# Kernel tuning notes

Hardware: AMD Instinct MI355X
Metric: run time of the kernel (lower is better)

Reference implementation:

```python
import jax, jax.numpy as jnp
import numpy as np

WIN_SIZE = 11
SIGMA = 1.5
WEIGHTS = np.array([0.0448, 0.2856, 0.3001, 0.2363, 0.1333], dtype=np.float32)
K1, K2 = 0.01, 0.03
DATA_RANGE = 255.0
C1 = (K1 * DATA_RANGE) ** 2
C2 = (K2 * DATA_RANGE) ** 2
N_SCALES = 5


def _gauss1d():
    coords = np.arange(WIN_SIZE, dtype=np.float32) - WIN_SIZE // 2
    g = np.exp(-(coords ** 2) / (2.0 * SIGMA ** 2))
    g /= g.sum()
    return jnp.asarray(g, dtype=jnp.float32)


def _blur(x, g):
    # separable depthwise gaussian blur, VALID padding (matches pytorch_msssim)
    C = x.shape[1]
    wh = jnp.tile(g.reshape(1, 1, 1, WIN_SIZE), (C, 1, 1, 1))
    wv = jnp.tile(g.reshape(1, 1, WIN_SIZE, 1), (C, 1, 1, 1))
    dn = ('NCHW', 'OIHW', 'NCHW')
    x = jax.lax.conv_general_dilated(x, wh, (1, 1), 'VALID', dimension_numbers=dn, feature_group_count=C)
    x = jax.lax.conv_general_dilated(x, wv, (1, 1), 'VALID', dimension_numbers=dn, feature_group_count=C)
    return x


def _ssim(X, Y, g):
    mu1 = _blur(X, g)
    mu2 = _blur(Y, g)
    mu1_sq = mu1 * mu1
    mu2_sq = mu2 * mu2
    mu1_mu2 = mu1 * mu2
    sigma1_sq = _blur(X * X, g) - mu1_sq
    sigma2_sq = _blur(Y * Y, g) - mu2_sq
    sigma12 = _blur(X * Y, g) - mu1_mu2
    cs_map = (2.0 * sigma12 + C2) / (sigma1_sq + sigma2_sq + C2)
    ssim_map = ((2.0 * mu1_mu2 + C1) / (mu1_sq + mu2_sq + C1)) * cs_map
    return ssim_map.mean(axis=(2, 3)), cs_map.mean(axis=(2, 3))  # [B,C] each


def _avg_pool2(x):
    # avg_pool2d kernel=2 stride=2; H,W chosen even at every scale so padding=0
    return jax.lax.reduce_window(x, 0.0, jax.lax.add, (1, 1, 2, 2), (1, 1, 2, 2), 'VALID') / 4.0


def setup_inputs() -> dict:
    key = jax.random.key(0)
    k1, k2 = jax.random.split(key)
    shape = (32, 3, 384, 384)
    prediction = jax.random.uniform(k1, shape, dtype=jnp.float32) * DATA_RANGE
    truth = jax.random.uniform(k2, shape, dtype=jnp.float32) * DATA_RANGE
    return {"prediction": prediction, "truth": truth}


def reference(prediction, truth):
    g = _gauss1d()
    w = jnp.asarray(WEIGHTS)
    X, Y = prediction, truth
    mcs = []
    for i in range(N_SCALES):
        ssim_pc, cs = _ssim(X, Y, g)
        if i < N_SCALES - 1:
            mcs.append(jax.nn.relu(cs))
            X = _avg_pool2(X)
            Y = _avg_pool2(Y)
    vals = jnp.stack(mcs + [jax.nn.relu(ssim_pc)], axis=0)  # [5,B,C]
    ms_ssim_val = jnp.prod(vals ** w.reshape(-1, 1, 1), axis=0)  # [B,C]
    return 1.0 - ms_ssim_val.mean()
```

## Files before the change

### kernel.cpp

```cpp
#include <hip/hip_runtime.h>
#include <math.h>


namespace {

constexpr int NIMG = 96;
constexpr float TWO_C1 = 13.005f;
constexpr float TWO_C2 = 117.045f;

__device__ constexpr float GW[11] = {
    0.00102838f, 0.00759875f, 0.03600077f, 0.10936070f, 0.21300553f,
    0.26601172f,
    0.21300553f, 0.10936070f, 0.03600077f, 0.00759875f, 0.00102838f};

typedef float f2 __attribute__((ext_vector_type(2)));
typedef float f4 __attribute__((ext_vector_type(4)));

__device__ __forceinline__ f2 pk_mul(f2 a, f2 b) {
  f2 d;
  asm("v_pk_mul_f32 %0, %1, %2" : "=v"(d) : "v"(a), "v"(b));
  return d;
}
__device__ __forceinline__ f2 pk_mul_s1lo(f2 a, f2 b) {
  f2 d;
  asm("v_pk_mul_f32 %0, %1, %2 op_sel:[0,0] op_sel_hi:[1,0]"
      : "=v"(d) : "v"(a), "v"(b));
  return d;
}
__device__ __forceinline__ void fma_w(f2& d, f2 q, f2 p) {
  asm("v_pk_fma_f32 %0, %1, %2, %0 op_sel:[0,0,0] op_sel_hi:[0,1,1]"
      : "+v"(d) : "v"(q), "v"(p));
}
__device__ __forceinline__ void fma_nl(f2& d, f2 q, f2 t) {
  asm("v_pk_fma_f32 %0, %1, %2, %0 op_sel:[0,0,0] op_sel_hi:[1,0,1]"
      : "+v"(d) : "v"(q), "v"(t));
}
__device__ __forceinline__ void fma_nh(f2& d, f2 q, f2 t) {
  asm("v_pk_fma_f32 %0, %1, %2, %0 op_sel:[0,1,0] op_sel_hi:[1,1,1]"
      : "+v"(d) : "v"(q), "v"(t));
}
__device__ __forceinline__ void fma_sl(f2& d, f2 q, f2 t) {
  asm("v_pk_fma_f32 %0, %1, %2, %0 op_sel:[1,0,0] op_sel_hi:[0,0,1]"
      : "+v"(d) : "v"(q), "v"(t));
}
__device__ __forceinline__ void fma_sh(f2& d, f2 q, f2 t) {
  asm("v_pk_fma_f32 %0, %1, %2, %0 op_sel:[1,1,0] op_sel_hi:[0,1,1]"
      : "+v"(d) : "v"(q), "v"(t));
}

__device__ __forceinline__ float wshl1(float v) {
  return __int_as_float(__builtin_amdgcn_mov_dpp(
      __float_as_int(v), 0x130, 0xF, 0xF, true));
}
__device__ __forceinline__ f2 wshl1v(f2 v) {
  f2 r;
  r.x = wshl1(v.x);
  r.y = wshl1(v.y);
  return r;
}

struct SPtrs {
  const float* ip[4];
};

template <bool BASE, bool CLAMP>
__device__ __forceinline__ void vblur(const float* __restrict__ XP,
                                      const float* __restrict__ YP, int row0,
                                      int W2, int H, int cp, f2 (&AU)[4],
                                      f2 (&AW)[4], f2 (&BU)[4], f2 (&BW)[4],
                                      const f2 (&QQ)[6]) {
  const f2* PA = (const f2*)XP;
  const f2* PB = (const f2*)YP;
  const f4* PV = (const f4*)XP;
  f2 sa[14], sb[14];
  f4 sv[14];
#pragma unroll
  for (int j = 0; j < 14; ++j) {
    int rin = row0 + j;
    if (CLAMP) rin = rin < H - 1 ? rin : H - 1;
    const int off = rin * W2 + cp;
    if (BASE) {
      sa[j] = PA[off];
      sb[j] = PB[off];
    } else {
      sv[j] = PV[off];
    }
  }
  __builtin_amdgcn_sched_barrier(0);
#pragma unroll
  for (int j = 0; j < 14; ++j) {
    f2 Pu, Pw;
    if (BASE) {
      f2 pa = sa[j], pb = sb[j];
      Pu = pa + pb;
      Pw = pa - pb;
    } else {
      f4 v = sv[j];
      Pu.x = v.x; Pu.y = v.y;
      Pw.x = v.z; Pw.y = v.w;
    }
    f2 Qu = pk_mul(Pu, Pu), Qw = pk_mul(Pw, Pw);
#pragma unroll
    for (int i = 0; i < 4; ++i) {
      const int k = j - i;
      if (k >= 0 && k <= 10) {
        const int qi = k <= 5 ? k : 10 - k;
        fma_w(AU[i], QQ[qi], Pu);
        fma_w(AW[i], QQ[qi], Pw);
        fma_w(BU[i], QQ[qi], Qu);
        fma_w(BW[i], QQ[qi], Qw);
      }
    }
  }
}

template <bool BASE>
__device__ __forceinline__ void ssim_tile(const float* __restrict__ XP,
                                          const float* __restrict__ YP,
                                          int H, int x0, int tw, int by,
                                          int s, int img,
                                          float* __restrict__ acc) {
  __shared__ float red[2][4];
  const int W2 = H >> 1, OH = H - 10;
  const int t = threadIdx.x;
  const int lane = t & 63, wv = t >> 6;
  int cp = (x0 >> 1) + lane;
  cp = cp < W2 - 1 ? cp : W2 - 1;
  const int row0 = by * 16 + wv * 4;

  f2 QQ[6];
  QQ[0].x = GW[0]; QQ[0].y = 0.f;
#pragma unroll
  for (int n = 1; n < 6; ++n) { QQ[n].x = GW[n]; QQ[n].y = GW[n - 1]; }

  float ssim_s = 0.f, cs_s = 0.f;

  if (row0 < OH) {
    f2 AU[4] = {}, AW[4] = {}, BU[4] = {}, BW[4] = {};
    const bool noclamp = (row0 + 13 <= H - 1);
    if (noclamp) vblur<BASE, false>(XP, YP, row0, W2, H, cp, AU, AW, BU, BW, QQ);
    else         vblur<BASE, true >(XP, YP, row0, W2, H, cp, AU, AW, BU, BW, QQ);

    auto hb = [&QQ](f2 tt) -> f2 {
      f2 h = pk_mul_s1lo(QQ[0], tt);
      fma_nh(h, QQ[1], tt);
      tt = wshl1v(tt);
      fma_nl(h, QQ[2], tt);
      fma_nh(h, QQ[3], tt);
      tt = wshl1v(tt);
      fma_nl(h, QQ[4], tt);
      fma_nh(h, QQ[5], tt);
      tt = wshl1v(tt);
      fma_sl(h, QQ[5], tt);
      fma_sh(h, QQ[4], tt);
      tt = wshl1v(tt);
      fma_sl(h, QQ[3], tt);
      fma_sh(h, QQ[2], tt);
      tt = wshl1v(tt);
      fma_sl(h, QQ[1], tt);
      fma_sh(h, QQ[0], tt);
      return h;
    };

    const bool vx = (2 * lane) < tw;
    const bool vy = (2 * lane + 1) < tw;
#pragma unroll
    for (int i = 0; i < 4; ++i) {
      if (row0 + i < OH) {
        f2 bU = hb(AU[i]), bW = hb(AW[i]);
        f2 bU2 = hb(BU[i]), bW2 = hb(BW[i]);
        f2 m2u = pk_mul(bU, bU), m2w = pk_mul(bW, bW);
        f2 Pm = m2u - m2w;
        f2 Qm = m2u + m2w;
        f2 Am = bU2 - bW2;
        f2 Bm = bU2 + bW2;
        float csx = (Am.x - Pm.x + TWO_C2) *
                    __builtin_amdgcn_rcpf(Bm.x - Qm.x + TWO_C2);
        float lx = (Pm.x + TWO_C1) * __builtin_amdgcn_rcpf(Qm.x + TWO_C1);
        float csy = (Am.y - Pm.y + TWO_C2) *
                    __builtin_amdgcn_rcpf(Bm.y - Qm.y + TWO_C2);
        float ly = (Pm.y + TWO_C1) * __builtin_amdgcn_rcpf(Qm.y + TWO_C1);
        if (vx) { cs_s += csx; ssim_s += lx * csx; }
        if (vy) { cs_s += csy; ssim_s += ly * csy; }
      }
    }
  }

#pragma unroll
  for (int off = 32; off > 0; off >>= 1) {
    ssim_s += __shfl_down(ssim_s, off);
    cs_s += __shfl_down(cs_s, off);
  }
  if (lane == 0) { red[0][wv] = ssim_s; red[1][wv] = cs_s; }
  __syncthreads();
  if (t == 0) {
    atomicAdd(&acc[(2 * s + 0) * NIMG + img],
              red[0][0] + red[0][1] + red[0][2] + red[0][3]);
    atomicAdd(&acc[(2 * s + 1) * NIMG + img],
              red[1][0] + red[1][1] + red[1][2] + red[1][3]);
  }
}

__device__ __forceinline__ void pyramid_body(
    const float* __restrict__ X, const float* __restrict__ Y,
    float* __restrict__ i1, float* __restrict__ i2,
    float* __restrict__ i3, float* __restrict__ i4, int img, int bx) {
  const int t = threadIdx.x;
  const int wv = t >> 6, lane = t & 63;
  const int tidx = bx * 4 + wv;
  const int tx = tidx % 6, ty = tidx / 6;
  const int r = lane >> 4, c = lane & 15;

  const float* Xs = X + (size_t)img * 384 * 384;
  const float* Ys = Y + (size_t)img * 384 * 384;
  f4* p1 = (f4*)i1 + (size_t)img * 192 * 96;
  f4* p2 = (f4*)i2 + (size_t)img * 96 * 48;
  f4* p3 = (f4*)i3 + (size_t)img * 48 * 24;
  f4* p4 = (f4*)i4 + (size_t)img * 24 * 12;

  float h4u = 0.f, h4w = 0.f;
#pragma unroll
  for (int b = 0; b < 2; ++b) {
    const int gr = ty * 16 + b * 8 + 2 * r;
    const int gc = tx * 64 + 4 * c;
    f4 xu = *(const f4*)&Xs[(size_t)gr * 384 + gc];
    f4 xv = *(const f4*)&Xs[(size_t)(gr + 1) * 384 + gc];
    f4 yu = *(const f4*)&Ys[(size_t)gr * 384 + gc];
    f4 yv = *(const f4*)&Ys[(size_t)(gr + 1) * 384 + gc];
    float ax = 0.25f * (xu.x + xu.y + xv.x + xv.y);
    float bx2 = 0.25f * (xu.z + xu.w + xv.z + xv.w);
    float ay = 0.25f * (yu.x + yu.y + yv.x + yv.y);
    float by2 = 0.25f * (yu.z + yu.w + yv.z + yv.w);
    float u0 = ax + ay, u1v = bx2 + by2, w0 = ax - ay, w1v = bx2 - by2;
    {
      f4 st; st.x = u0; st.y = u1v; st.z = w0; st.w = w1v;
      p1[(size_t)(ty * 8 + b * 4 + r) * 96 + tx * 16 + c] = st;
    }
    float hu = u0 + u1v, hw = w0 + w1v;
    float su = 0.25f * (hu + __shfl_xor(hu, 16));
    float sw = 0.25f * (hw + __shfl_xor(hw, 16));
    float suh = __shfl_xor(su, 1), swh = __shfl_xor(sw, 1);
    if ((r & 1) == 0 && (c & 1) == 0) {
      f4 st; st.x = su; st.y = suh; st.z = sw; st.w = swh;
      p2[(size_t)(ty * 4 + 2 * b + (r >> 1)) * 48 + tx * 8 + (c >> 1)] = st;
    }
    float au = su + __shfl_xor(su, 1);
    float aw = sw + __shfl_xor(sw, 1);
    float u3 = 0.25f * (au + __shfl_xor(au, 32));
    float w3 = 0.25f * (aw + __shfl_xor(aw, 32));
    float u3h = __shfl_xor(u3, 2), w3h = __shfl_xor(w3, 2);
    if (r == 0 && (c & 3) == 0) {
      f4 st; st.x = u3; st.y = u3h; st.z = w3; st.w = w3h;
      p3[(size_t)(ty * 2 + b) * 24 + tx * 4 + (c >> 2)] = st;
    }
    float hu4 = u3 + __shfl_xor(u3, 2);
    float hw4 = w3 + __shfl_xor(w3, 2);
    if (b == 0) {
      h4u = hu4; h4w = hw4;
    } else {
      float l4u = 0.25f * (h4u + hu4), l4w = 0.25f * (h4w + hw4);
      float l4uh = __shfl_xor(l4u, 4), l4wh = __shfl_xor(l4w, 4);
      if (r == 0 && (c & 7) == 0) {
        f4 st; st.x = l4u; st.y = l4uh; st.z = l4w; st.w = l4wh;
        p4[(size_t)ty * 12 + tx * 2 + (c >> 3)] = st;
      }
    }
  }
}

__global__ __launch_bounds__(256, 4) void fused_pyr_s0(
    const float* __restrict__ X, const float* __restrict__ Y,
    float* __restrict__ i1, float* __restrict__ i2,
    float* __restrict__ i3, float* __restrict__ i4,
    float* __restrict__ acc) {
  const int img = blockIdx.y;
  if (blockIdx.x < 36) {
    pyramid_body(X, Y, i1, i2, i3, i4, img, blockIdx.x);
    return;
  }
  const int lt = blockIdx.x - 36;
  const int tx = lt & 3, by = lt >> 2;
  const int x0 = tx * 94;
  int tw = 374 - x0;
  tw = tw < 94 ? tw : 94;
  ssim_tile<true>(X + (size_t)img * 384 * 384, Y + (size_t)img * 384 * 384,
                  384, x0, tw, by, 0, img, acc);
}

__global__ __launch_bounds__(256, 4) void ssim_rest(SPtrs sp,
                                                    float* __restrict__ acc) {
  const int img = blockIdx.y;
  const int tile = 96 + blockIdx.x;
  int s;
  if (tile < 120) s = 1;
  else if (tile < 126) s = 2;
  else if (tile < 129) s = 3;
  else s = 4;
  const int tstart[5] = {0, 96, 120, 126, 129};
  const int HH[5] = {384, 192, 96, 48, 24};
  const int NTX[5] = {4, 2, 1, 1, 1};
  const int TWM[5] = {94, 92, 86, 38, 14};
  const int lt = tile - tstart[s];
  const int H = HH[s], OW = H - 10;
  const int tx = lt % NTX[s], by = lt / NTX[s];
  const int x0 = tx * TWM[s];
  const int tw = (TWM[s] < OW - x0) ? TWM[s] : OW - x0;
  const float* XP = sp.ip[s - 1] + (size_t)img * H * (H >> 1) * 4;
  ssim_tile<false>(XP, nullptr, H, x0, tw, by, s, img, acc);
}

__global__ void final_kernel(const float* __restrict__ acc,
                             float* __restrict__ out) {
  __shared__ float prods[NIMG];
  const float wts[5] = {0.0448f, 0.2856f, 0.3001f, 0.2363f, 0.1333f};
  const float inv_npix[5] = {1.f / (374.f * 374.f), 1.f / (182.f * 182.f),
                             1.f / (86.f * 86.f),  1.f / (38.f * 38.f),
                             1.f / (14.f * 14.f)};
  int t = threadIdx.x;
  if (t < NIMG) {
    float p = 1.f;
#pragma unroll
    for (int s = 0; s < 5; ++s) {
      float sum = (s < 4) ? acc[(s * 2 + 1) * NIMG + t]
                          : acc[(s * 2 + 0) * NIMG + t];
      float m = sum * inv_npix[s];
      m = m > 0.f ? m : 0.f;
      p *= powf(m, wts[s]);
    }
    prods[t] = p;
  }
  __syncthreads();
  if (t == 0) {
    float s = 0.f;
    for (int i = 0; i < NIMG; ++i) s += prods[i];
    out[0] = 1.f - s / (float)NIMG;
  }
}

}

extern "C" void kernel_launch(void* const* d_in, const int* in_sizes, int n_in,
                              void* d_out, int out_size, void* d_ws,
                              size_t ws_size, hipStream_t stream) {
  const float* X0 = (const float*)d_in[0];
  const float* Y0 = (const float*)d_in[1];
  float* out = (float*)d_out;
  float* ws = (float*)d_ws;

  const size_t L1 = (size_t)NIMG * 192 * 192 * 2;
  const size_t L2 = (size_t)NIMG * 96 * 96 * 2;
  const size_t L3 = (size_t)NIMG * 48 * 48 * 2;
  const size_t L4 = (size_t)NIMG * 24 * 24 * 2;

  float* i1 = ws;
  float* i2 = i1 + L1;
  float* i3 = i2 + L2;
  float* i4 = i3 + L3;
  float* acc = i4 + L4;

  hipMemsetAsync(acc, 0, 10 * NIMG * sizeof(float), stream);

  fused_pyr_s0<<<dim3(36 + 96, NIMG), dim3(256), 0, stream>>>(
      X0, Y0, i1, i2, i3, i4, acc);

  SPtrs sp;
  sp.ip[0] = i1; sp.ip[1] = i2; sp.ip[2] = i3; sp.ip[3] = i4;

  ssim_rest<<<dim3(34, NIMG), dim3(256), 0, stream>>>(sp, acc);

  final_kernel<<<dim3(1), dim3(128), 0, stream>>>(acc, out);
}
```

Before: 221.3 us.

## Halve vblur load buffer, raise occupancy bound, fold final reduction into last block

The vertical blur now prefetches only 7 rows into registers and refills slots as rows are consumed, instead of preloading all 14. This lowers register pressure so both main kernels can request 5 waves per SIMD instead of 4. The separate final kernel launch is removed: ssim_rest blocks increment an atomic counter, and the last block computes the MS-SSIM product and mean. The smaller prefetch window exposes more load latency, and the tail now depends on atomics and fences working correctly.

```diff
diff --git a/kernel.cpp b/kernel.cpp
--- a/kernel.cpp
+++ b/kernel.cpp
@@ -7,6 +7,7 @@
 constexpr int NIMG = 96;
 constexpr float TWO_C1 = 13.005f;
 constexpr float TWO_C2 = 117.045f;
+constexpr int TOTAL_B = 34 * NIMG;
 
 __device__ constexpr float GW[11] = {
     0.00102838f, 0.00759875f, 0.03600077f, 0.10936070f, 0.21300553f,
@@ -72,10 +73,10 @@
   const f2* PA = (const f2*)XP;
   const f2* PB = (const f2*)YP;
   const f4* PV = (const f4*)XP;
-  f2 sa[14], sb[14];
-  f4 sv[14];
-#pragma unroll
-  for (int j = 0; j < 14; ++j) {
+  f2 sa[7], sb[7];
+  f4 sv[7];
+#pragma unroll
+  for (int j = 0; j < 7; ++j) {
     int rin = row0 + j;
     if (CLAMP) rin = rin < H - 1 ? rin : H - 1;
     const int off = rin * W2 + cp;
@@ -91,13 +92,24 @@
   for (int j = 0; j < 14; ++j) {
     f2 Pu, Pw;
     if (BASE) {
-      f2 pa = sa[j], pb = sb[j];
+      f2 pa = sa[j % 7], pb = sb[j % 7];
       Pu = pa + pb;
       Pw = pa - pb;
     } else {
-      f4 v = sv[j];
+      f4 v = sv[j % 7];
       Pu.x = v.x; Pu.y = v.y;
       Pw.x = v.z; Pw.y = v.w;
+    }
+    if (j + 7 < 14) {
+      int rin = row0 + j + 7;
+      if (CLAMP) rin = rin < H - 1 ? rin : H - 1;
+      const int off = rin * W2 + cp;
+      if (BASE) {
+        sa[j % 7] = PA[off];
+        sb[j % 7] = PB[off];
+      } else {
+        sv[j % 7] = PV[off];
+      }
     }
     f2 Qu = pk_mul(Pu, Pu), Qw = pk_mul(Pw, Pw);
 #pragma unroll
@@ -268,7 +280,7 @@
   }
 }
 
-__global__ __launch_bounds__(256, 4) void fused_pyr_s0(
+__global__ __launch_bounds__(256, 5) void fused_pyr_s0(
     const float* __restrict__ X, const float* __restrict__ Y,
     float* __restrict__ i1, float* __restrict__ i2,
     float* __restrict__ i3, float* __restrict__ i4,
@@ -287,8 +299,10 @@
                   384, x0, tw, by, 0, img, acc);
 }
 
-__global__ __launch_bounds__(256, 4) void ssim_rest(SPtrs sp,
-                                                    float* __restrict__ acc) {
+__global__ __launch_bounds__(256, 5) void ssim_rest(SPtrs sp,
+                                                    float* __restrict__ acc,
+                                                    int* __restrict__ ctr,
+                                                    float* __restrict__ out) {
   const int img = blockIdx.y;
   const int tile = 96 + blockIdx.x;
   int s;
@@ -307,33 +321,41 @@
   const int tw = (TWM[s] < OW - x0) ? TWM[s] : OW - x0;
   const float* XP = sp.ip[s - 1] + (size_t)img * H * (H >> 1) * 4;
   ssim_tile<false>(XP, nullptr, H, x0, tw, by, s, img, acc);
-}
-
-__global__ void final_kernel(const float* __restrict__ acc,
-                             float* __restrict__ out) {
-  __shared__ float prods[NIMG];
-  const float wts[5] = {0.0448f, 0.2856f, 0.3001f, 0.2363f, 0.1333f};
-  const float inv_npix[5] = {1.f / (374.f * 374.f), 1.f / (182.f * 182.f),
-                             1.f / (86.f * 86.f),  1.f / (38.f * 38.f),
-                             1.f / (14.f * 14.f)};
-  int t = threadIdx.x;
-  if (t < NIMG) {
-    float p = 1.f;
-#pragma unroll
-    for (int s = 0; s < 5; ++s) {
-      float sum = (s < 4) ? acc[(s * 2 + 1) * NIMG + t]
-                          : acc[(s * 2 + 0) * NIMG + t];
-      float m = sum * inv_npix[s];
-      m = m > 0.f ? m : 0.f;
-      p *= powf(m, wts[s]);
-    }
-    prods[t] = p;
+
+  const int t = threadIdx.x;
+  __shared__ int sh_last;
+  if (t == 0) {
+    __threadfence();
+    int old = atomicAdd(ctr, 1);
+    sh_last = (old == TOTAL_B - 1) ? 1 : 0;
   }
   __syncthreads();
-  if (t == 0) {
-    float s = 0.f;
-    for (int i = 0; i < NIMG; ++i) s += prods[i];
-    out[0] = 1.f - s / (float)NIMG;
+  if (sh_last) {
+    __threadfence();
+    __shared__ float prods[NIMG];
+    const float wts[5] = {0.0448f, 0.2856f, 0.3001f, 0.2363f, 0.1333f};
+    const float inv_npix[5] = {1.f / (374.f * 374.f), 1.f / (182.f * 182.f),
+                               1.f / (86.f * 86.f),  1.f / (38.f * 38.f),
+                               1.f / (14.f * 14.f)};
+    if (t < NIMG) {
+      const volatile float* vacc = acc;
+      float p = 1.f;
+#pragma unroll
+      for (int q = 0; q < 5; ++q) {
+        float sum = (q < 4) ? vacc[(q * 2 + 1) * NIMG + t]
+                            : vacc[(q * 2 + 0) * NIMG + t];
+        float m = sum * inv_npix[q];
+        m = m > 0.f ? m : 0.f;
+        p *= powf(m, wts[q]);
+      }
+      prods[t] = p;
+    }
+    __syncthreads();
+    if (t == 0) {
+      float sm = 0.f;
+      for (int i = 0; i < NIMG; ++i) sm += prods[i];
+      out[0] = 1.f - sm / (float)NIMG;
+    }
   }
 }
 
@@ -357,8 +379,9 @@
   float* i3 = i2 + L2;
   float* i4 = i3 + L3;
   float* acc = i4 + L4;
-
-  hipMemsetAsync(acc, 0, 10 * NIMG * sizeof(float), stream);
+  int* ctr = (int*)(acc + 10 * NIMG);
+
+  hipMemsetAsync(acc, 0, (10 * NIMG + 1) * sizeof(float), stream);
 
   fused_pyr_s0<<<dim3(36 + 96, NIMG), dim3(256), 0, stream>>>(
       X0, Y0, i1, i2, i3, i4, acc);
@@ -366,7 +389,5 @@
   SPtrs sp;
   sp.ip[0] = i1; sp.ip[1] = i2; sp.ip[2] = i3; sp.ip[3] = i4;
 
-  ssim_rest<<<dim3(34, NIMG), dim3(256), 0, stream>>>(sp, acc);
-
-  final_kernel<<<dim3(1), dim3(128), 0, stream>>>(acc, out);
-}
+  ssim_rest<<<dim3(34, NIMG), dim3(256), 0, stream>>>(sp, acc, ctr, out);
+}
```

Result: slower. 303.7 us (+37.2%).
